# Optimization experiments

Hardware: AMD Instinct MI355X
Metric: run time of the kernel (lower is better)

Reference implementation:

```python
import jax, jax.numpy as jnp
import numpy as np

EPS = 1e-5

def _bn_relu(y, mean, var, scale, bias):
    # y: (b, c, n); eval-mode batchnorm over channel axis, then ReLU
    inv = scale / jnp.sqrt(var + EPS)
    return jax.nn.relu((y - mean[None, :, None]) * inv[None, :, None] + bias[None, :, None])

def setup_inputs() -> dict:
    key = jax.random.key(0)
    ks = jax.random.split(key, 6)
    b, c, n, cr = 4, 256, 4096, 32
    inp = {
        'x': jax.random.normal(ks[0], (b, c, n), jnp.float32),
        'w_q': jax.random.normal(ks[1], (cr, c), jnp.float32) * (1.0 / np.sqrt(c)),
        'w_k': jax.random.normal(ks[2], (cr, c), jnp.float32) * (1.0 / np.sqrt(c)),
        'w_v': jax.random.normal(ks[3], (c, c), jnp.float32) * (1.0 / np.sqrt(c)),
        'bn1_scale': jnp.ones((cr,), jnp.float32), 'bn1_bias': jnp.zeros((cr,), jnp.float32),
        'bn1_mean': jnp.zeros((cr,), jnp.float32), 'bn1_var': jnp.ones((cr,), jnp.float32),
        'bn2_scale': jnp.ones((cr,), jnp.float32), 'bn2_bias': jnp.zeros((cr,), jnp.float32),
        'bn2_mean': jnp.zeros((cr,), jnp.float32), 'bn2_var': jnp.ones((cr,), jnp.float32),
        'bn3_scale': jnp.ones((c,), jnp.float32), 'bn3_bias': jnp.zeros((c,), jnp.float32),
        'bn3_mean': jnp.zeros((c,), jnp.float32), 'bn3_var': jnp.ones((c,), jnp.float32),
        'gamma': jax.random.normal(ks[4], (1,), jnp.float32),
    }
    return inp

def reference(x, w_q, w_k, w_v,
              bn1_scale, bn1_bias, bn1_mean, bn1_var,
              bn2_scale, bn2_bias, bn2_mean, bn2_var,
              bn3_scale, bn3_bias, bn3_mean, bn3_var,
              gamma):
    # x: (b, c, n). Original views as (b, c, n, 1) so width=1, height=n.
    b, c, n = x.shape
    # 1x1 conv == channel matmul, then BN+ReLU
    q = _bn_relu(jnp.einsum('oc,bcn->bon', w_q, x), bn1_mean, bn1_var, bn1_scale, bn1_bias)  # (b, c', n)
    k = _bn_relu(jnp.einsum('oc,bcn->bon', w_k, x), bn2_mean, bn2_var, bn2_scale, bn2_bias)  # (b, c', n)
    v = _bn_relu(jnp.einsum('oc,bcn->bon', w_v, x), bn3_mean, bn3_var, bn3_scale, bn3_bias)  # (b, c, n)
    # energy_H: (b, n, n) with -inf diagonal (self-attention along 'height')
    energy_h = jnp.einsum('bdi,bdj->bij', q, k)
    eye = jnp.eye(n, dtype=bool)
    energy_h = jnp.where(eye[None], -jnp.inf, energy_h)
    # energy_W: width=1 -> per-position self energy (b, n)
    energy_w = jnp.sum(q * k, axis=1)
    # softmax over concat of n H-logits and 1 W-logit
    att = jax.nn.softmax(jnp.concatenate([energy_h, energy_w[..., None]], axis=-1), axis=-1)  # (b, n, n+1)
    att_h = att[..., :n]        # (b, n, n), query i -> key j
    att_w = att[..., n]         # (b, n)
    out_h = jnp.einsum('bcj,bij->bci', v, att_h)   # aggregate values along height
    out_w = v * att_w[:, None, :]                  # width=1 self term
    out = gamma[0] * (out_h + out_w) + x
    return out
```

## Files before the change

### kernel.cpp

```cpp
#include <hip/hip_runtime.h>

#define Bb 4
#define Cc 256
#define Nn 4096
#define CR 32
#define EPS_BN 1e-5f
#define SHIFT2 28.853900817779268f
#define LOG2E  1.4426950408889634f
#define JSPLIT 4
#define JSL (Nn / JSPLIT)
#define TJ 64
#define NTILES (JSL / TJ)

typedef __attribute__((ext_vector_type(8))) short short8;
typedef __attribute__((ext_vector_type(4))) float f32x4;

__device__ inline unsigned int pk2(float a, float b) {
    __bf16 ha = (__bf16)a, hb = (__bf16)b;
    unsigned short ra = __builtin_bit_cast(unsigned short, ha);
    unsigned short rb = __builtin_bit_cast(unsigned short, hb);
    return ((unsigned int)rb << 16) | ra;
}
__device__ inline float blo(unsigned int u) { return __uint_as_float(u << 16); }
__device__ inline float bhi(unsigned int u) { return __uint_as_float(u & 0xffff0000u); }
__device__ inline float ex2(float x) { return __builtin_amdgcn_exp2f(x); }

__global__ __launch_bounds__(256) void prep_w(
    const float* __restrict__ wq, const float* __restrict__ wk,
    const float* __restrict__ wv, __bf16* __restrict__ Wf)
{
    const int r16 = blockIdx.x;
    const int tid = threadIdx.x;
#pragma unroll
    for (int ss = 0; ss < 2; ++ss) {
        int s = tid + ss * 256;
        int kc = s >> 6, lane = s & 63;
        int R = r16 * 16 + (lane & 15);
        const float* src = (R < 32) ? (wq + (size_t)R * Cc)
                         : (R < 64) ? (wk + (size_t)(R - 32) * Cc)
                                    : (wv + (size_t)(R - 64) * Cc);
        const float* p = src + kc * 32 + (lane >> 4) * 8;
        float4 a = *(const float4*)p;
        float4 c2 = *(const float4*)(p + 4);
        uint4 pk = { pk2(a.x,a.y), pk2(a.z,a.w), pk2(c2.x,c2.y), pk2(c2.z,c2.w) };
        *(uint4*)&Wf[(((size_t)r16 * 8 + kc) * 64 + lane) * 8] = pk;
    }
}

__global__ __launch_bounds__(256) void qkv_kernel(
    const float* __restrict__ x, const __bf16* __restrict__ Wf,
    const float* __restrict__ bn1s, const float* __restrict__ bn1b, const float* __restrict__ bn1m, const float* __restrict__ bn1v,
    const float* __restrict__ bn2s, const float* __restrict__ bn2b, const float* __restrict__ bn2m, const float* __restrict__ bn2v,
    const float* __restrict__ bn3s, const float* __restrict__ bn3b, const float* __restrict__ bn3m, const float* __restrict__ bn3v,
    __bf16* __restrict__ Qt, __bf16* __restrict__ Kt, __bf16* __restrict__ Vb)
{
    __shared__ __align__(16) float  sXf[4][32 * 40];
    __shared__ __align__(16) __bf16 sXt[4][2][32 * 40];
    __shared__ __align__(16) __bf16 oT[128 * 136];

    const int tid = threadIdx.x;
    const int n0 = blockIdx.x * 128, g = blockIdx.y, b = blockIdx.z;
    const int lane = tid & 63, w = tid >> 6;
    const int l15 = lane & 15, l4 = lane >> 4;
    const int nmt = (g == 0) ? 4 : 8;
    const int r16b = (g == 0) ? 0 : 4 + (g - 1) * 8;

    float*  sXfw  = &sXf[w][0];
    __bf16* sXtw0 = &sXt[w][0][0];
    __bf16* sXtw1 = &sXt[w][1][0];

    const int cr = lane >> 3, nq = lane & 7;
    const float* xbase = x + (size_t)(b * Cc + cr) * Nn + n0 + w * 32 + nq * 4;

    float4 xg[4];
#pragma unroll
    for (int it = 0; it < 4; ++it)
        xg[it] = *(const float4*)&xbase[(size_t)(it * 8) * Nn];

    f32x4 acc[8][2];
#pragma unroll
    for (int mt = 0; mt < 8; ++mt)
#pragma unroll
        for (int nt = 0; nt < 2; ++nt) acc[mt][nt] = (f32x4){0.f, 0.f, 0.f, 0.f};

    for (int kc = 0; kc < 8; ++kc) {
#pragma unroll
        for (int it = 0; it < 4; ++it)
            *(float4*)&sXfw[(it * 8 + cr) * 40 + nq * 4] = xg[it];

        if (kc + 1 < 8) {
#pragma unroll
            for (int it = 0; it < 4; ++it)
                xg[it] = *(const float4*)&xbase[(size_t)((kc + 1) * 32 + it * 8) * Nn];
        }

#pragma unroll
        for (int s = 0; s < 2; ++s) {
            int n = lane & 31, c0 = (lane >> 5) * 8 + s * 16;
            float h[8], lo[8];
#pragma unroll
            for (int j = 0; j < 8; ++j) {
                float v = sXfw[(c0 + j) * 40 + n];
                float hh = (float)(__bf16)v;
                h[j] = hh; lo[j] = v - hh;
            }
            uint4 H = { pk2(h[0],h[1]), pk2(h[2],h[3]), pk2(h[4],h[5]), pk2(h[6],h[7]) };
            uint4 L = { pk2(lo[0],lo[1]), pk2(lo[2],lo[3]), pk2(lo[4],lo[5]), pk2(lo[6],lo[7]) };
            *(uint4*)&sXtw0[n * 40 + c0] = H;
            *(uint4*)&sXtw1[n * 40 + c0] = L;
        }

        short8 bh[2], bl[2];
#pragma unroll
        for (int nt = 0; nt < 2; ++nt) {
            bh[nt] = *(const short8*)&sXtw0[(nt * 16 + l15) * 40 + l4 * 8];
            bl[nt] = *(const short8*)&sXtw1[(nt * 16 + l15) * 40 + l4 * 8];
        }
        short8 af[8];
#pragma unroll
        for (int mt = 0; mt < 8; ++mt)
            if (mt < nmt)
                af[mt] = *(const short8*)&Wf[(((size_t)(r16b + mt) * 8 + kc) * 64 + lane) * 8];
#pragma unroll
        for (int mt = 0; mt < 8; ++mt) {
            if (mt < nmt) {
#pragma unroll
                for (int nt = 0; nt < 2; ++nt) {
                    acc[mt][nt] = __builtin_amdgcn_mfma_f32_16x16x32_bf16(af[mt], bh[nt], acc[mt][nt], 0, 0, 0);
                    acc[mt][nt] = __builtin_amdgcn_mfma_f32_16x16x32_bf16(af[mt], bl[nt], acc[mt][nt], 0, 0, 0);
                }
            }
        }
    }

    if (g == 0) {
#pragma unroll
        for (int mt = 0; mt < 4; ++mt) {
            float scl[4], off[4];
#pragma unroll
            for (int r = 0; r < 4; ++r) {
                int R = mt * 16 + l4 * 4 + r;
                float s, o;
                if (R < 32) {
                    s = bn1s[R] * __frsqrt_rn(bn1v[R] + EPS_BN);
                    o = bn1b[R] - bn1m[R] * s;
                } else {
                    int row = R - 32;
                    s = bn2s[row] * __frsqrt_rn(bn2v[row] + EPS_BN);
                    o = bn2b[row] - bn2m[row] * s;
                    s *= LOG2E; o *= LOG2E;
                }
                scl[r] = s; off[r] = o;
            }
            __bf16* dst = (mt < 2) ? Qt : Kt;
            int d0 = (mt & 1) * 16 + l4 * 4;
#pragma unroll
            for (int nt = 0; nt < 2; ++nt) {
                f32x4 a = acc[mt][nt];
                float e0 = fmaxf(fmaf(a.x, scl[0], off[0]), 0.f);
                float e1 = fmaxf(fmaf(a.y, scl[1], off[1]), 0.f);
                float e2 = fmaxf(fmaf(a.z, scl[2], off[2]), 0.f);
                float e3 = fmaxf(fmaf(a.w, scl[3], off[3]), 0.f);
                uint2 p = { pk2(e0, e1), pk2(e2, e3) };
                int n = n0 + w * 32 + nt * 16 + l15;
                *(uint2*)&dst[(size_t)(b * Nn + n) * CR + d0] = p;
            }
        }
    } else {
        const int vr0 = (g - 1) * 128;
#pragma unroll
        for (int mt = 0; mt < 8; ++mt) {
            float scl[4], off[4];
#pragma unroll
            for (int r = 0; r < 4; ++r) {
                int row = vr0 + mt * 16 + l4 * 4 + r;
                float s = bn3s[row] * __frsqrt_rn(bn3v[row] + EPS_BN);
                scl[r] = s; off[r] = bn3b[row] - bn3m[row] * s;
            }
#pragma unroll
            for (int nt = 0; nt < 2; ++nt) {
                f32x4 a = acc[mt][nt];
                float e[4];
                e[0] = fmaxf(fmaf(a.x, scl[0], off[0]), 0.f);
                e[1] = fmaxf(fmaf(a.y, scl[1], off[1]), 0.f);
                e[2] = fmaxf(fmaf(a.z, scl[2], off[2]), 0.f);
                e[3] = fmaxf(fmaf(a.w, scl[3], off[3]), 0.f);
                int ncol = w * 32 + nt * 16 + l15;
#pragma unroll
                for (int r = 0; r < 4; ++r)
                    oT[(mt * 16 + l4 * 4 + r) * 136 + ncol] = (__bf16)e[r];
            }
        }
        __syncthreads();
        int rr = tid >> 1, qq = tid & 1;
        size_t vrow = (size_t)(b * Cc + vr0 + rr) * Nn + n0 + qq * 64;
#pragma unroll
        for (int e8 = 0; e8 < 8; ++e8)
            *(uint4*)&Vb[vrow + e8 * 8] = *(const uint4*)&oT[rr * 136 + qq * 64 + e8 * 8];
    }
}

__global__ __launch_bounds__(256) void attn_kernel(
    const __bf16* __restrict__ Qt, const __bf16* __restrict__ Kt,
    const __bf16* __restrict__ Vb,
    __bf16* __restrict__ PO, float* __restrict__ PL)
{
    __shared__ __align__(16) __bf16 sQ[64 * 40];
    __shared__ __align__(16) __bf16 sP[2][64 * 72];
    __shared__ __align__(16) float  sL[4][64];

    const int tid = threadIdx.x, lane = tid & 63, w = tid >> 6;
    const int b = blockIdx.z, js = blockIdx.y, iblk = blockIdx.x;
    const int i0 = iblk * 64;
    const int l15 = lane & 15, l4 = lane >> 4;

    {
        int i = tid >> 2, o = tid & 3;
        *(uint4*)&sQ[i * 40 + o * 8] =
            *(const uint4*)&Qt[(size_t)(b * Nn + i0 + i) * CR + o * 8];
    }
    __syncthreads();
    short8 qf[4];
#pragma unroll
    for (int it = 0; it < 4; ++it)
        qf[it] = *(const short8*)&sQ[(it * 16 + l15) * 40 + l4 * 8];

    f32x4 oacc[16];
#pragma unroll
    for (int z = 0; z < 16; ++z) oacc[z] = (f32x4){0.f, 0.f, 0.f, 0.f};
    float lp[4] = {0.f, 0.f, 0.f, 0.f};

    const size_t jb = (size_t)js * JSL;

    short8 kf = *(const short8*)&Kt[(size_t)(b * Nn + jb + 16 * w + l15) * CR + l4 * 8];

    short8 vf[8];
#pragma unroll
    for (int u = 0; u < 8; ++u) {
        int jh = u >> 2, ct = u & 3;
        int c = w * 64 + ct * 16 + l15;
        vf[u] = *(const short8*)&Vb[(size_t)(b * Cc + c) * Nn + jb + (jh * 4 + l4) * 8];
    }

#pragma unroll
    for (int it = 0; it < 4; ++it) {
        f32x4 c0 = (f32x4){0.f, 0.f, 0.f, 0.f};
        c0 = __builtin_amdgcn_mfma_f32_16x16x32_bf16(kf, qf[it], c0, 0, 0, 0);
        float e0 = ex2(c0.x - SHIFT2), e1 = ex2(c0.y - SHIFT2);
        float e2 = ex2(c0.z - SHIFT2), e3 = ex2(c0.w - SHIFT2);
        lp[it] += (e0 + e1) + (e2 + e3);
        uint2 p2 = { pk2(e0, e1), pk2(e2, e3) };
        *(uint2*)&sP[0][(it * 16 + l15) * 72 + w * 16 + l4 * 4] = p2;
    }
    kf = *(const short8*)&Kt[(size_t)(b * Nn + jb + TJ + 16 * w + l15) * CR + l4 * 8];
    __syncthreads();

    for (int t = 0; t < NTILES; ++t) {
        const size_t j0 = jb + (size_t)t * TJ;
        const __bf16* sPr = &sP[t & 1][0];
        __bf16*       sPn = &sP[(t + 1) & 1][0];

        if (t + 1 < NTILES) {
#pragma unroll
            for (int it = 0; it < 4; ++it) {
                f32x4 c0 = (f32x4){0.f, 0.f, 0.f, 0.f};
                c0 = __builtin_amdgcn_mfma_f32_16x16x32_bf16(kf, qf[it], c0, 0, 0, 0);
                float e0 = ex2(c0.x - SHIFT2), e1 = ex2(c0.y - SHIFT2);
                float e2 = ex2(c0.z - SHIFT2), e3 = ex2(c0.w - SHIFT2);
                lp[it] += (e0 + e1) + (e2 + e3);
                uint2 p2 = { pk2(e0, e1), pk2(e2, e3) };
                *(uint2*)&sPn[(it * 16 + l15) * 72 + w * 16 + l4 * 4] = p2;
            }
        }

        __builtin_amdgcn_s_setprio(1);
#pragma unroll
        for (int jh = 0; jh < 2; ++jh) {
            short8 pf[4];
#pragma unroll
            for (int it = 0; it < 4; ++it)
                pf[it] = *(const short8*)&sPr[(it * 16 + l15) * 72 + jh * 32 + l4 * 8];
#pragma unroll
            for (int ct = 0; ct < 4; ++ct) {
#pragma unroll
                for (int it = 0; it < 4; ++it)
                    oacc[it * 4 + ct] = __builtin_amdgcn_mfma_f32_16x16x32_bf16(
                        pf[it], vf[jh * 4 + ct], oacc[it * 4 + ct], 0, 0, 0);
            }
        }
        __builtin_amdgcn_s_setprio(0);

        if (t + 1 < NTILES) {
#pragma unroll
            for (int u = 0; u < 8; ++u) {
                int jh = u >> 2, ct = u & 3;
                int c = w * 64 + ct * 16 + l15;
                vf[u] = *(const short8*)&Vb[(size_t)(b * Cc + c) * Nn + j0 + TJ + (jh * 4 + l4) * 8];
            }
            if (t + 2 < NTILES)
                kf = *(const short8*)&Kt[(size_t)(b * Nn + j0 + 2 * TJ + 16 * w + l15) * CR + l4 * 8];
            __syncthreads();
        }
    }

#pragma unroll
    for (int it = 0; it < 4; ++it) {
        float v = lp[it];
        v += __shfl_xor(v, 16);
        v += __shfl_xor(v, 32);
        if (lane < 16) sL[w][it * 16 + lane] = v;
    }
    __syncthreads();
    if (tid < 64)
        PL[(size_t)(js * Bb + b) * Nn + i0 + tid] =
            sL[0][tid] + sL[1][tid] + sL[2][tid] + sL[3][tid];

    const size_t base = (size_t)((js * Bb + b) * (Nn / 64) + iblk) * 16384;
#pragma unroll
    for (int it = 0; it < 4; ++it)
#pragma unroll
        for (int ct = 0; ct < 4; ++ct) {
            f32x4 a = oacc[it * 4 + ct];
            uint2 p = { pk2(a.x, a.y), pk2(a.z, a.w) };
            *(uint2*)&PO[base + (size_t)((((w * 4 + it) * 4 + ct) * 64 + lane)) * 4] = p;
        }
}

__global__ __launch_bounds__(256) void reduce_kernel(
    const __bf16* __restrict__ PO, const float* __restrict__ PL,
    const float* __restrict__ x, const float* __restrict__ gamma,
    float* __restrict__ out)
{
    __shared__ __align__(16) float oT[64 * 68];
    __shared__ float sLinv[64];

    const int tid = threadIdx.x;
    const int iblk = blockIdx.x, wq = blockIdx.y, b = blockIdx.z;
    const int i0 = iblk * 64;
    const int lane = tid & 63, ct = tid >> 6, l15 = lane & 15, l4 = lane >> 4;

    if (tid < 64) {
        float l = 0.f;
#pragma unroll
        for (int js = 0; js < JSPLIT; ++js)
            l += PL[(size_t)(js * Bb + b) * Nn + i0 + tid];
        sLinv[tid] = 1.0f / l;
    }

    float o[4][4];
#pragma unroll
    for (int it = 0; it < 4; ++it) {
        o[it][0] = o[it][1] = o[it][2] = o[it][3] = 0.f;
#pragma unroll
        for (int js = 0; js < JSPLIT; ++js) {
            size_t base = (size_t)((js * Bb + b) * (Nn / 64) + iblk) * 16384;
            uint2 v = *(const uint2*)&PO[base + (size_t)((((wq * 4 + it) * 4 + ct) * 64 + lane)) * 4];
            o[it][0] += blo(v.x); o[it][1] += bhi(v.x);
            o[it][2] += blo(v.y); o[it][3] += bhi(v.y);
        }
    }

    const int cl = ct * 16 + l15;
#pragma unroll
    for (int it = 0; it < 4; ++it) {
        float4 t4 = { o[it][0], o[it][1], o[it][2], o[it][3] };
        *(float4*)&oT[cl * 68 + it * 16 + l4 * 4] = t4;
    }
    __syncthreads();

    const float g = gamma[0];
    const int c_l = tid >> 2, icol = (tid & 3) * 16;
    const int cg = wq * 64 + c_l;
    const size_t gb = (size_t)(b * Cc + cg) * Nn + i0 + icol;
#pragma unroll
    for (int k4 = 0; k4 < 4; ++k4) {
        float4 ov = *(const float4*)&oT[c_l * 68 + icol + k4 * 4];
        float4 li = *(const float4*)&sLinv[icol + k4 * 4];
        float4 xv = *(const float4*)&x[gb + k4 * 4];
        float4 res;
        res.x = fmaf(g, ov.x * li.x, xv.x);
        res.y = fmaf(g, ov.y * li.y, xv.y);
        res.z = fmaf(g, ov.z * li.z, xv.z);
        res.w = fmaf(g, ov.w * li.w, xv.w);
        *(float4*)&out[gb + k4 * 4] = res;
    }
}

extern "C" void kernel_launch(void* const* d_in, const int* in_sizes, int n_in,
                              void* d_out, int out_size, void* d_ws, size_t ws_size,
                              hipStream_t stream)
{
    const float* x    = (const float*)d_in[0];
    const float* wq   = (const float*)d_in[1];
    const float* wk   = (const float*)d_in[2];
    const float* wv   = (const float*)d_in[3];
    const float* bn1s = (const float*)d_in[4];
    const float* bn1b = (const float*)d_in[5];
    const float* bn1m = (const float*)d_in[6];
    const float* bn1v = (const float*)d_in[7];
    const float* bn2s = (const float*)d_in[8];
    const float* bn2b = (const float*)d_in[9];
    const float* bn2m = (const float*)d_in[10];
    const float* bn2v = (const float*)d_in[11];
    const float* bn3s = (const float*)d_in[12];
    const float* bn3b = (const float*)d_in[13];
    const float* bn3m = (const float*)d_in[14];
    const float* bn3v = (const float*)d_in[15];
    const float* gmm  = (const float*)d_in[16];
    float* out = (float*)d_out;

    char* ws = (char*)d_ws;
    __bf16* Qt  = (__bf16*)(ws);
    __bf16* Kt  = (__bf16*)(ws + (1u << 20));
    __bf16* Vb  = (__bf16*)(ws + (2u << 20));
    char*   big = ws + (10u << 20);
    __bf16* PO  = (__bf16*)big;
    float*  PL  = (float*)(big + 33554432);
    __bf16* Wf  = (__bf16*)(big + 33554432 + 262144);

    prep_w<<<dim3(20), 256, 0, stream>>>(wq, wk, wv, Wf);

    qkv_kernel<<<dim3(Nn / 128, 3, Bb), 256, 0, stream>>>(
        x, Wf,
        bn1s, bn1b, bn1m, bn1v,
        bn2s, bn2b, bn2m, bn2v,
        bn3s, bn3b, bn3m, bn3v,
        Qt, Kt, Vb);

    attn_kernel<<<dim3(Nn / 64, JSPLIT, Bb), 256, 0, stream>>>(Qt, Kt, Vb, PO, PL);

    reduce_kernel<<<dim3(Nn / 64, 4, Bb), 256, 0, stream>>>(PO, PL, x, gmm, out);
}
```

Before: 204.4 us.

## Split attention channels across two blocks, single-buffer P, raise occupancy

The attention kernel now splits the 256 value channels into two halves handled by separate blocks, doubling the grid and halving each block's accumulators and V fragments. It drops the double-buffered P tile and software prefetch in favour of a simpler per-tile load, compute, sync loop, and adds a launch-bounds occupancy hint of 4. The aim is lower register pressure and more resident waves to hide latency. The cost is that QK^T and exp are computed twice per tile (once per channel half), plus an extra barrier per tile and less explicit overlap of loads with compute.

```diff
diff --git a/kernel.cpp b/kernel.cpp
--- a/kernel.cpp
+++ b/kernel.cpp
@@ -200,18 +200,19 @@
     }
 }
 
-__global__ __launch_bounds__(256) void attn_kernel(
+__global__ __launch_bounds__(256, 4) void attn_kernel(
     const __bf16* __restrict__ Qt, const __bf16* __restrict__ Kt,
     const __bf16* __restrict__ Vb,
     __bf16* __restrict__ PO, float* __restrict__ PL)
 {
     __shared__ __align__(16) __bf16 sQ[64 * 40];
-    __shared__ __align__(16) __bf16 sP[2][64 * 72];
+    __shared__ __align__(16) __bf16 sP[64 * 72];
     __shared__ __align__(16) float  sL[4][64];
 
     const int tid = threadIdx.x, lane = tid & 63, w = tid >> 6;
-    const int b = blockIdx.z, js = blockIdx.y, iblk = blockIdx.x;
-    const int i0 = iblk * 64;
+    const int b = blockIdx.z, iblk = blockIdx.x;
+    const int js = blockIdx.y & 3, ch = blockIdx.y >> 2;
+    const int i0 = iblk * 64, cb = ch * 128;
     const int l15 = lane & 15, l4 = lane >> 4;
 
     {
@@ -225,53 +226,42 @@
     for (int it = 0; it < 4; ++it)
         qf[it] = *(const short8*)&sQ[(it * 16 + l15) * 40 + l4 * 8];
 
-    f32x4 oacc[16];
-#pragma unroll
-    for (int z = 0; z < 16; ++z) oacc[z] = (f32x4){0.f, 0.f, 0.f, 0.f};
+    f32x4 oacc[8];
+#pragma unroll
+    for (int z = 0; z < 8; ++z) oacc[z] = (f32x4){0.f, 0.f, 0.f, 0.f};
     float lp[4] = {0.f, 0.f, 0.f, 0.f};
 
     const size_t jb = (size_t)js * JSL;
-
     short8 kf = *(const short8*)&Kt[(size_t)(b * Nn + jb + 16 * w + l15) * CR + l4 * 8];
 
-    short8 vf[8];
-#pragma unroll
-    for (int u = 0; u < 8; ++u) {
-        int jh = u >> 2, ct = u & 3;
-        int c = w * 64 + ct * 16 + l15;
-        vf[u] = *(const short8*)&Vb[(size_t)(b * Cc + c) * Nn + jb + (jh * 4 + l4) * 8];
-    }
-
-#pragma unroll
-    for (int it = 0; it < 4; ++it) {
-        f32x4 c0 = (f32x4){0.f, 0.f, 0.f, 0.f};
-        c0 = __builtin_amdgcn_mfma_f32_16x16x32_bf16(kf, qf[it], c0, 0, 0, 0);
-        float e0 = ex2(c0.x - SHIFT2), e1 = ex2(c0.y - SHIFT2);
-        float e2 = ex2(c0.z - SHIFT2), e3 = ex2(c0.w - SHIFT2);
-        lp[it] += (e0 + e1) + (e2 + e3);
-        uint2 p2 = { pk2(e0, e1), pk2(e2, e3) };
-        *(uint2*)&sP[0][(it * 16 + l15) * 72 + w * 16 + l4 * 4] = p2;
-    }
-    kf = *(const short8*)&Kt[(size_t)(b * Nn + jb + TJ + 16 * w + l15) * CR + l4 * 8];
-    __syncthreads();
+    const __bf16* vrow0 = Vb + (size_t)(b * Cc + cb + w * 32 + l15) * Nn;
 
     for (int t = 0; t < NTILES; ++t) {
         const size_t j0 = jb + (size_t)t * TJ;
-        const __bf16* sPr = &sP[t & 1][0];
-        __bf16*       sPn = &sP[(t + 1) & 1][0];
-
-        if (t + 1 < NTILES) {
-#pragma unroll
-            for (int it = 0; it < 4; ++it) {
-                f32x4 c0 = (f32x4){0.f, 0.f, 0.f, 0.f};
-                c0 = __builtin_amdgcn_mfma_f32_16x16x32_bf16(kf, qf[it], c0, 0, 0, 0);
-                float e0 = ex2(c0.x - SHIFT2), e1 = ex2(c0.y - SHIFT2);
-                float e2 = ex2(c0.z - SHIFT2), e3 = ex2(c0.w - SHIFT2);
-                lp[it] += (e0 + e1) + (e2 + e3);
-                uint2 p2 = { pk2(e0, e1), pk2(e2, e3) };
-                *(uint2*)&sPn[(it * 16 + l15) * 72 + w * 16 + l4 * 4] = p2;
-            }
-        }
+
+        short8 vf[4];
+#pragma unroll
+        for (int u = 0; u < 4; ++u) {
+            int jh = u >> 1, ct = u & 1;
+            vf[u] = *(const short8*)&vrow0[(size_t)(ct * 16) * Nn + j0 + jh * 32 + l4 * 8];
+        }
+
+#pragma unroll
+        for (int it = 0; it < 4; ++it) {
+            f32x4 c0 = (f32x4){0.f, 0.f, 0.f, 0.f};
+            c0 = __builtin_amdgcn_mfma_f32_16x16x32_bf16(kf, qf[it], c0, 0, 0, 0);
+            float e0 = ex2(c0.x - SHIFT2);
+            float e1 = ex2(c0.y - SHIFT2);
+            float e2 = ex2(c0.z - SHIFT2);
+            float e3 = ex2(c0.w - SHIFT2);
+            lp[it] += (e0 + e1) + (e2 + e3);
+            uint2 p2 = { pk2(e0, e1), pk2(e2, e3) };
+            *(uint2*)&sP[(it * 16 + l15) * 72 + w * 16 + l4 * 4] = p2;
+        }
+        __syncthreads();
+
+        if (t + 1 < NTILES)
+            kf = *(const short8*)&Kt[(size_t)(b * Nn + j0 + TJ + 16 * w + l15) * CR + l4 * 8];
 
         __builtin_amdgcn_s_setprio(1);
 #pragma unroll
@@ -279,28 +269,17 @@
             short8 pf[4];
 #pragma unroll
             for (int it = 0; it < 4; ++it)
-                pf[it] = *(const short8*)&sPr[(it * 16 + l15) * 72 + jh * 32 + l4 * 8];
-#pragma unroll
-            for (int ct = 0; ct < 4; ++ct) {
+                pf[it] = *(const short8*)&sP[(it * 16 + l15) * 72 + jh * 32 + l4 * 8];
+#pragma unroll
+            for (int ct = 0; ct < 2; ++ct) {
 #pragma unroll
                 for (int it = 0; it < 4; ++it)
-                    oacc[it * 4 + ct] = __builtin_amdgcn_mfma_f32_16x16x32_bf16(
-                        pf[it], vf[jh * 4 + ct], oacc[it * 4 + ct], 0, 0, 0);
+                    oacc[it * 2 + ct] = __builtin_amdgcn_mfma_f32_16x16x32_bf16(
+                        pf[it], vf[jh * 2 + ct], oacc[it * 2 + ct], 0, 0, 0);
             }
         }
         __builtin_amdgcn_s_setprio(0);
-
-        if (t + 1 < NTILES) {
-#pragma unroll
-            for (int u = 0; u < 8; ++u) {
-                int jh = u >> 2, ct = u & 3;
-                int c = w * 64 + ct * 16 + l15;
-                vf[u] = *(const short8*)&Vb[(size_t)(b * Cc + c) * Nn + j0 + TJ + (jh * 4 + l4) * 8];
-            }
-            if (t + 2 < NTILES)
-                kf = *(const short8*)&Kt[(size_t)(b * Nn + j0 + 2 * TJ + 16 * w + l15) * CR + l4 * 8];
-            __syncthreads();
-        }
+        __syncthreads();
     }
 
 #pragma unroll
@@ -311,7 +290,7 @@
         if (lane < 16) sL[w][it * 16 + lane] = v;
     }
     __syncthreads();
-    if (tid < 64)
+    if (ch == 0 && tid < 64)
         PL[(size_t)(js * Bb + b) * Nn + i0 + tid] =
             sL[0][tid] + sL[1][tid] + sL[2][tid] + sL[3][tid];
 
@@ -319,10 +298,12 @@
 #pragma unroll
     for (int it = 0; it < 4; ++it)
 #pragma unroll
-        for (int ct = 0; ct < 4; ++ct) {
-            f32x4 a = oacc[it * 4 + ct];
+        for (int ct = 0; ct < 2; ++ct) {
+            f32x4 a = oacc[it * 2 + ct];
             uint2 p = { pk2(a.x, a.y), pk2(a.z, a.w) };
-            *(uint2*)&PO[base + (size_t)((((w * 4 + it) * 4 + ct) * 64 + lane)) * 4] = p;
+            int g16 = ch * 8 + w * 2 + ct;
+            int s = (g16 >> 2) * 16 + it * 4 + (g16 & 3);
+            *(uint2*)&PO[base + (size_t)(s * 64 + lane) * 4] = p;
         }
 }
 
@@ -427,7 +408,7 @@
         bn3s, bn3b, bn3m, bn3v,
         Qt, Kt, Vb);
 
-    attn_kernel<<<dim3(Nn / 64, JSPLIT, Bb), 256, 0, stream>>>(Qt, Kt, Vb, PO, PL);
+    attn_kernel<<<dim3(Nn / 64, JSPLIT * 2, Bb), 256, 0, stream>>>(Qt, Kt, Vb, PO, PL);
 
     reduce_kernel<<<dim3(Nn / 64, 4, Bb), 256, 0, stream>>>(PO, PL, x, gmm, out);
 }
```

Result: slower. 209.8 us (+2.6%).
